# Performance work log

Hardware: AMD Instinct MI355X
Metric: run time of the kernel (lower is better)

## Reference

```python
import jax, jax.numpy as jnp
import numpy as np

TAU = 0.07
EPS = 1e-6  # torch CosineSimilarity eps


def setup_inputs() -> dict:
    key = jax.random.key(0)
    k1, k2, k3 = jax.random.split(key, 3)
    n, d, n_classes = 8192, 256, 1024
    imitation_embeds = jax.random.normal(k1, (n, d), dtype=jnp.float32)
    recording_embeds = jax.random.normal(k2, (n, d), dtype=jnp.float32)
    labels = jax.random.randint(k3, (n,), 0, n_classes, dtype=jnp.int64)
    return {
        "imitation_embeds": imitation_embeds,
        "recording_embeds": recording_embeds,
        "labels": labels,
    }


def reference(imitation_embeds, recording_embeds, labels):
    n = imitation_embeds.shape[0]
    # cosine similarity with per-vector norm clamp (torch semantics)
    im_n = imitation_embeds / jnp.maximum(
        jnp.linalg.norm(imitation_embeds, axis=1, keepdims=True), EPS)
    rec_n = recording_embeds / jnp.maximum(
        jnp.linalg.norm(recording_embeds, axis=1, keepdims=True), EPS)
    i2r = jnp.einsum("nd,md->nm", im_n, rec_n) / TAU  # [n, n]

    same = labels[:, None] == labels[None, :]          # [n, n] bool
    eye = jnp.eye(n, dtype=bool)
    # original: mask = ~(same ^ diag_embed(diag(same))); diag(same) is all True
    # -> keep the diagonal (positive) and all different-label negatives
    mask = ~(same ^ eye)

    # per-row masked log-softmax evaluated at the diagonal entry:
    # log_softmax(row[mask])[pos_of_diag] = i2r[i,i] - logsumexp(row over mask)
    lse = jax.nn.logsumexp(jnp.where(mask, i2r, -jnp.inf), axis=1)  # [n]
    loss = -jnp.mean(jnp.diagonal(i2r) - lse)
    return loss
```

## Files before the change

### kernel.cpp

```cpp
#include <hip/hip_runtime.h>

#define N 8192
#define D 256
#define INV_TAU 14.285714285714286f
#define LOG2E 1.4426950408889634f
#define EPSN 1e-6f

#define RT 256
#define CT 64
#define CSPLIT 16
#define CPB (N / CSPLIT)
#define NTILES (CPB / CT)
#define MAXC 96

typedef unsigned int u32x4 __attribute__((ext_vector_type(4)));
typedef __bf16 bf16x8 __attribute__((ext_vector_type(8)));
typedef float f32x4 __attribute__((ext_vector_type(4)));

__device__ inline unsigned short f2bf(float x) {
    unsigned int u = __builtin_bit_cast(unsigned int, x);
    u += 0x7fffu + ((u >> 16) & 1u);
    return (unsigned short)(u >> 16);
}

__device__ inline float bf2f(unsigned short u) {
    return __builtin_bit_cast(float, (unsigned int)u << 16);
}

__global__ void ntx_prep(const float* __restrict__ im, const float* __restrict__ rec,
                         unsigned short* __restrict__ A, unsigned short* __restrict__ Bm,
                         float* __restrict__ diag, float* __restrict__ rowsum,
                         int* __restrict__ cnt, float* __restrict__ out) {
    const int wave = threadIdx.x >> 6;
    const int lane = threadIdx.x & 63;
    const int row  = blockIdx.x * 4 + wave;

    const float4 a = ((const float4*)(im  + (size_t)row * D))[lane];
    const float4 b = ((const float4*)(rec + (size_t)row * D))[lane];

    float ssa = a.x*a.x + a.y*a.y + a.z*a.z + a.w*a.w;
    float ssb = b.x*b.x + b.y*b.y + b.z*b.z + b.w*b.w;
    float dt  = a.x*b.x + a.y*b.y + a.z*b.z + a.w*b.w;
    #pragma unroll
    for (int o = 32; o; o >>= 1) {
        ssa += __shfl_xor(ssa, o);
        ssb += __shfl_xor(ssb, o);
        dt  += __shfl_xor(dt , o);
    }
    const float ra = 1.0f / fmaxf(sqrtf(ssa), EPSN);
    const float rb = 1.0f / fmaxf(sqrtf(ssb), EPSN);
    const float sa = ra * (INV_TAU * LOG2E);

    ushort4 pa, pb;
    pa.x = f2bf(a.x*sa); pa.y = f2bf(a.y*sa); pa.z = f2bf(a.z*sa); pa.w = f2bf(a.w*sa);
    pb.x = f2bf(b.x*rb); pb.y = f2bf(b.y*rb); pb.z = f2bf(b.z*rb); pb.w = f2bf(b.w*rb);
    *(ushort4*)(A  + (size_t)row * D + lane * 4) = pa;
    *(ushort4*)(Bm + (size_t)row * D + lane * 4) = pb;

    if (lane == 0) {
        diag[row]   = dt * ra * rb * INV_TAU;
        rowsum[row] = 0.0f;
    }
    if (blockIdx.x < 4) cnt[blockIdx.x * 256 + threadIdx.x] = 0;
    if (blockIdx.x == 0 && threadIdx.x == 0) out[0] = 0.0f;
}

__global__ void ntx_bucket(const int* __restrict__ labels, int* __restrict__ cnt,
                           int* __restrict__ bucket) {
    const int i = blockIdx.x * 256 + threadIdx.x;
    const int c = labels[i];
    const int pos = atomicAdd(&cnt[c], 1);
    if (pos < MAXC) bucket[c * MAXC + pos] = i;
}

__global__ void ntx_pairs(const unsigned short* __restrict__ A,
                          const unsigned short* __restrict__ Bm,
                          const int* __restrict__ labels,
                          const int* __restrict__ cnt, const int* __restrict__ bucket,
                          float* __restrict__ rowsum) {
    const int wave = threadIdx.x >> 6;
    const int lane = threadIdx.x & 63;
    const int i = blockIdx.x * 4 + wave;
    const int c = labels[i];
    const int m = min(cnt[c], MAXC);
    if (m < 2) return;

    const ushort4 av = *(const ushort4*)(A + (size_t)i * D + lane * 4);
    const float a0 = bf2f(av.x), a1 = bf2f(av.y), a2 = bf2f(av.z), a3 = bf2f(av.w);

    int jr_n = bucket[c * MAXC];
    ushort4 bv_n = *(const ushort4*)(Bm + (size_t)jr_n * D + lane * 4);

    float corr = 0.f;
    for (int j = 0; j < m; ++j) {
        const int jr = jr_n;
        const ushort4 bv = bv_n;
        if (j + 1 < m) {
            jr_n = bucket[c * MAXC + j + 1];
            bv_n = *(const ushort4*)(Bm + (size_t)jr_n * D + lane * 4);
        }
        if (jr == i) continue;
        float d = a0*bf2f(bv.x) + a1*bf2f(bv.y) + a2*bf2f(bv.z) + a3*bf2f(bv.w);
        #pragma unroll
        for (int o = 32; o; o >>= 1) d += __shfl_xor(d, o);
        corr += __builtin_amdgcn_exp2f(d);
    }
    if (lane == 0) atomicAdd(&rowsum[i], -corr);
}

__device__ __forceinline__ void stage_tile(const unsigned short* gs, unsigned char* lb) {
    #pragma unroll
    for (int p = 0; p < 8; ++p)
        __builtin_amdgcn_global_load_lds(
            (const __attribute__((address_space(1))) unsigned int*)(gs + p * 32),
            (__attribute__((address_space(3))) unsigned int*)(lb + p * 1024),
            16, 0, 0);
}

__global__ __launch_bounds__(256, 2)
void ntx_lse(const unsigned short* __restrict__ A, const unsigned short* __restrict__ Bm,
             float* __restrict__ rowsum) {
    __shared__ __align__(128) unsigned char Bs[2][CT * 512];

    const int wave = threadIdx.x >> 6;
    const int lane = threadIdx.x & 63;
    const int g    = lane >> 4;
    const int n16  = lane & 15;

    const int rowblk = blockIdx.x & (N / RT - 1);
    const int colblk = blockIdx.x >> 5;
    const int row0 = rowblk * RT + wave * 64;
    const int col0 = colblk * CPB;

    bf16x8 afrag[4][8];
    #pragma unroll
    for (int rs = 0; rs < 4; ++rs) {
        const int r = row0 + rs * 16 + n16;
        #pragma unroll
        for (int k = 0; k < 8; ++k)
            afrag[rs][k] = __builtin_bit_cast(
                bf16x8, *(const u32x4*)(A + (size_t)r * D + k * 32 + g * 8));
    }

    float acc[4][4];
    #pragma unroll
    for (int rs = 0; rs < 4; ++rs)
        #pragma unroll
        for (int q = 0; q < 4; ++q) acc[rs][q] = 0.f;

    const unsigned short* gsrc0 = Bm + (size_t)(col0 + wave * 16 + n16) * D + g * 8;
    unsigned char* lds0 = &Bs[0][wave * 8192];
    unsigned char* lds1 = &Bs[1][wave * 8192];

    stage_tile(gsrc0, lds0);
    asm volatile("s_waitcnt vmcnt(0)" ::: "memory");
    __builtin_amdgcn_s_barrier();
    __builtin_amdgcn_sched_barrier(0);

    for (int t = 0; t < NTILES; ++t) {
        const int buf = t & 1;
        if (t + 1 < NTILES)
            stage_tile(gsrc0 + (size_t)(t + 1) * CT * D, buf ? lds0 : lds1);

        #pragma unroll
        for (int cs = 0; cs < 4; ++cs) {
            bf16x8 bfrag[8];
            #pragma unroll
            for (int k = 0; k < 8; ++k)
                bfrag[k] = __builtin_bit_cast(
                    bf16x8, *(const u32x4*)(&Bs[buf][(cs * 8 + k) * 1024 + lane * 16]));

            #pragma unroll
            for (int rs = 0; rs < 4; ++rs) {
                f32x4 c = {0.f, 0.f, 0.f, 0.f};
                #pragma unroll
                for (int k = 0; k < 8; ++k)
                    c = __builtin_amdgcn_mfma_f32_16x16x32_bf16(
                            afrag[rs][k], bfrag[k], c, 0, 0, 0);
                #pragma unroll
                for (int q = 0; q < 4; ++q)
                    acc[rs][q] += __builtin_amdgcn_exp2f(c[q]);
            }
        }

        asm volatile("s_waitcnt vmcnt(0)" ::: "memory");
        __builtin_amdgcn_s_barrier();
        __builtin_amdgcn_sched_barrier(0);
    }

    #pragma unroll
    for (int rs = 0; rs < 4; ++rs)
        #pragma unroll
        for (int q = 0; q < 4; ++q) {
            float v = acc[rs][q];
            v += __shfl_xor(v, 1);
            v += __shfl_xor(v, 2);
            v += __shfl_xor(v, 4);
            v += __shfl_xor(v, 8);
            if (n16 == 0)
                atomicAdd(&rowsum[row0 + rs * 16 + g * 4 + q], v);
        }
}

__global__ void ntx_finish(const float* __restrict__ diag,
                           const float* __restrict__ rowsum,
                           float* __restrict__ out) {
    __shared__ float red[4];
    const int i = blockIdx.x * 256 + threadIdx.x;
    float s = logf(rowsum[i]) - diag[i];
    #pragma unroll
    for (int o = 32; o; o >>= 1) s += __shfl_xor(s, o);
    if ((threadIdx.x & 63) == 0) red[threadIdx.x >> 6] = s;
    __syncthreads();
    if (threadIdx.x == 0)
        atomicAdd(out, (red[0] + red[1] + red[2] + red[3]) * (1.0f / (float)N));
}

extern "C" void kernel_launch(void* const* d_in, const int* in_sizes, int n_in,
                              void* d_out, int out_size, void* d_ws, size_t ws_size,
                              hipStream_t stream) {
    const float* im     = (const float*)d_in[0];
    const float* rec    = (const float*)d_in[1];
    const int*   labels = (const int*)d_in[2];
    float* out = (float*)d_out;

    unsigned short* A  = (unsigned short*)d_ws;
    unsigned short* Bm = A + (size_t)N * D;
    float* diag   = (float*)(Bm + (size_t)N * D);
    float* rowsum = diag + N;
    int*   cnt    = (int*)(rowsum + N);
    int*   bucket = cnt + 1024;

    ntx_prep<<<N / 4, 256, 0, stream>>>(im, rec, A, Bm, diag, rowsum, cnt, out);
    ntx_bucket<<<N / 256, 256, 0, stream>>>(labels, cnt, bucket);
    ntx_pairs<<<N / 4, 256, 0, stream>>>(A, Bm, labels, cnt, bucket, rowsum);
    ntx_lse<<<(N / RT) * CSPLIT, 256, 0, stream>>>(A, Bm, rowsum);
    ntx_finish<<<N / 256, 256, 0, stream>>>(diag, rowsum, out);
}
```

Before: 121.8 us.

## Triple-buffer B tiles with smaller column tiles and interleaved async staging

The LSE GEMM kernel now uses 32-column tiles in a three-buffer LDS ring with two tiles prefetched, waiting with a partial vmcnt instead of draining all loads each iteration. Staging loads are interleaved into the compute sub-steps, all four row-slices' MFMAs are issued before the exp2 accumulation, and s_setprio raises wave priority around the MFMA block. The goal is to hide global-to-LDS latency and overlap matrix work with exponentials. In exchange there are twice as many barriers per column range and the scheduling is more complex.

```diff
diff --git a/kernel.cpp b/kernel.cpp
--- a/kernel.cpp
+++ b/kernel.cpp
@@ -7,7 +7,7 @@
 #define EPSN 1e-6f
 
 #define RT 256
-#define CT 64
+#define CT 32
 #define CSPLIT 16
 #define CPB (N / CSPLIT)
 #define NTILES (CPB / CT)
@@ -108,19 +108,73 @@
     if (lane == 0) atomicAdd(&rowsum[i], -corr);
 }
 
-__device__ __forceinline__ void stage_tile(const unsigned short* gs, unsigned char* lb) {
-    #pragma unroll
-    for (int p = 0; p < 8; ++p)
+__device__ __forceinline__ void stage_tile4(const unsigned short* __restrict__ Bm,
+                                            int colt, int wave, int lane,
+                                            unsigned char* lb) {
+    const int g = lane >> 4, n16 = lane & 15;
+    #pragma unroll
+    for (int p = 0; p < 4; ++p) {
+        const int csk = wave * 4 + p;
+        const int cs = csk >> 3, k = csk & 7;
+        const unsigned short* gs =
+            Bm + (size_t)(colt + cs * 16 + n16) * D + k * 32 + g * 8;
         __builtin_amdgcn_global_load_lds(
-            (const __attribute__((address_space(1))) unsigned int*)(gs + p * 32),
-            (__attribute__((address_space(3))) unsigned int*)(lb + p * 1024),
+            (const __attribute__((address_space(1))) unsigned int*)gs,
+            (__attribute__((address_space(3))) unsigned int*)(lb + csk * 1024),
             16, 0, 0);
+    }
+}
+
+template<bool STAGE>
+__device__ __forceinline__ void tile_step(const unsigned short* __restrict__ Bm,
+                                          int colstage, int wave, int lane,
+                                          const unsigned char* cur, unsigned char* stg,
+                                          const bf16x8 (&afrag)[4][8], float (&acc)[4][4]) {
+    const int g = lane >> 4, n16 = lane & 15;
+    #pragma unroll
+    for (int cs = 0; cs < 2; ++cs) {
+        if constexpr (STAGE) {
+            #pragma unroll
+            for (int p = cs * 2; p < cs * 2 + 2; ++p) {
+                const int csk = wave * 4 + p;
+                const int scs = csk >> 3, sk = csk & 7;
+                const unsigned short* gs =
+                    Bm + (size_t)(colstage + scs * 16 + n16) * D + sk * 32 + g * 8;
+                __builtin_amdgcn_global_load_lds(
+                    (const __attribute__((address_space(1))) unsigned int*)gs,
+                    (__attribute__((address_space(3))) unsigned int*)(stg + csk * 1024),
+                    16, 0, 0);
+            }
+        }
+        bf16x8 bfrag[8];
+        #pragma unroll
+        for (int k = 0; k < 8; ++k)
+            bfrag[k] = __builtin_bit_cast(
+                bf16x8, *(const u32x4*)(cur + (cs * 8 + k) * 1024 + lane * 16));
+
+        f32x4 c[4];
+        __builtin_amdgcn_s_setprio(1);
+        #pragma unroll
+        for (int rs = 0; rs < 4; ++rs) {
+            c[rs] = (f32x4){0.f, 0.f, 0.f, 0.f};
+            #pragma unroll
+            for (int k = 0; k < 8; ++k)
+                c[rs] = __builtin_amdgcn_mfma_f32_16x16x32_bf16(
+                            afrag[rs][k], bfrag[k], c[rs], 0, 0, 0);
+        }
+        __builtin_amdgcn_s_setprio(0);
+        #pragma unroll
+        for (int rs = 0; rs < 4; ++rs)
+            #pragma unroll
+            for (int q = 0; q < 4; ++q)
+                acc[rs][q] += __builtin_amdgcn_exp2f(c[rs][q]);
+    }
 }
 
 __global__ __launch_bounds__(256, 2)
 void ntx_lse(const unsigned short* __restrict__ A, const unsigned short* __restrict__ Bm,
              float* __restrict__ rowsum) {
-    __shared__ __align__(128) unsigned char Bs[2][CT * 512];
+    __shared__ __align__(128) unsigned char Bs[3][CT * 512];
 
     const int wave = threadIdx.x >> 6;
     const int lane = threadIdx.x & 63;
@@ -148,45 +202,29 @@
         #pragma unroll
         for (int q = 0; q < 4; ++q) acc[rs][q] = 0.f;
 
-    const unsigned short* gsrc0 = Bm + (size_t)(col0 + wave * 16 + n16) * D + g * 8;
-    unsigned char* lds0 = &Bs[0][wave * 8192];
-    unsigned char* lds1 = &Bs[1][wave * 8192];
-
-    stage_tile(gsrc0, lds0);
+    unsigned char* b0 = &Bs[0][0];
+    unsigned char* b1 = &Bs[1][0];
+    unsigned char* b2 = &Bs[2][0];
+
+    stage_tile4(Bm, col0,      wave, lane, b0);
+    stage_tile4(Bm, col0 + CT, wave, lane, b1);
+
+    for (int t = 0; t < NTILES - 1; ++t) {
+        asm volatile("s_waitcnt vmcnt(4)" ::: "memory");
+        __builtin_amdgcn_s_barrier();
+        __builtin_amdgcn_sched_barrier(0);
+
+        if (t + 2 < NTILES)
+            tile_step<true >(Bm, col0 + (t + 2) * CT, wave, lane, b0, b2, afrag, acc);
+        else
+            tile_step<false>(Bm, 0, wave, lane, b0, b2, afrag, acc);
+
+        unsigned char* tmp = b0; b0 = b1; b1 = b2; b2 = tmp;
+    }
     asm volatile("s_waitcnt vmcnt(0)" ::: "memory");
     __builtin_amdgcn_s_barrier();
     __builtin_amdgcn_sched_barrier(0);
-
-    for (int t = 0; t < NTILES; ++t) {
-        const int buf = t & 1;
-        if (t + 1 < NTILES)
-            stage_tile(gsrc0 + (size_t)(t + 1) * CT * D, buf ? lds0 : lds1);
-
-        #pragma unroll
-        for (int cs = 0; cs < 4; ++cs) {
-            bf16x8 bfrag[8];
-            #pragma unroll
-            for (int k = 0; k < 8; ++k)
-                bfrag[k] = __builtin_bit_cast(
-                    bf16x8, *(const u32x4*)(&Bs[buf][(cs * 8 + k) * 1024 + lane * 16]));
-
-            #pragma unroll
-            for (int rs = 0; rs < 4; ++rs) {
-                f32x4 c = {0.f, 0.f, 0.f, 0.f};
-                #pragma unroll
-                for (int k = 0; k < 8; ++k)
-                    c = __builtin_amdgcn_mfma_f32_16x16x32_bf16(
-                            afrag[rs][k], bfrag[k], c, 0, 0, 0);
-                #pragma unroll
-                for (int q = 0; q < 4; ++q)
-                    acc[rs][q] += __builtin_amdgcn_exp2f(c[q]);
-            }
-        }
-
-        asm volatile("s_waitcnt vmcnt(0)" ::: "memory");
-        __builtin_amdgcn_s_barrier();
-        __builtin_amdgcn_sched_barrier(0);
-    }
+    tile_step<false>(Bm, 0, wave, lane, b0, b2, afrag, acc);
 
     #pragma unroll
     for (int rs = 0; rs < 4; ++rs)
```

Measured after the change: 121.0 us. No clear change (-0.7%).

## Switch LSE kernel to per-wave double-buffered B tiles without block barriers

Applied to the files above, without the earlier changes.

Each wave now stages its own 16-column B tile into a private double buffer and waits only on its own outstanding loads (vmcnt), so the block-wide barriers after every tile go away. MFMAs are interleaved across the four row subtiles with raised scheduling priority, and the block-to-(row,column) mapping is reordered so neighbouring blocks share column ranges for better L2 reuse. The cost is smaller tiles, more issue overhead per tile, and a reliance on vmcnt ordering being correct for the global_load_lds path.

```diff
diff --git a/kernel.cpp b/kernel.cpp
--- a/kernel.cpp
+++ b/kernel.cpp
@@ -7,10 +7,11 @@
 #define EPSN 1e-6f
 
 #define RT 256
-#define CT 64
+#define CT 16
 #define CSPLIT 16
 #define CPB (N / CSPLIT)
 #define NTILES (CPB / CT)
+#define WTILE (CT * 512)
 #define MAXC 96
 
 typedef unsigned int u32x4 __attribute__((ext_vector_type(4)));
@@ -108,27 +109,67 @@
     if (lane == 0) atomicAdd(&rowsum[i], -corr);
 }
 
-__device__ __forceinline__ void stage_tile(const unsigned short* gs, unsigned char* lb) {
+__device__ __forceinline__ void stage_wtile(const unsigned short* __restrict__ Bm,
+                                            int colt, int lane, unsigned char* buf) {
+    const int g = lane >> 4, n16 = lane & 15;
+    const unsigned short* gs = Bm + (size_t)(colt + n16) * D + g * 8;
     #pragma unroll
     for (int p = 0; p < 8; ++p)
         __builtin_amdgcn_global_load_lds(
             (const __attribute__((address_space(1))) unsigned int*)(gs + p * 32),
-            (__attribute__((address_space(3))) unsigned int*)(lb + p * 1024),
+            (__attribute__((address_space(3))) unsigned int*)(buf + p * 1024),
             16, 0, 0);
+}
+
+template<int W, bool STG>
+__device__ __forceinline__ void wtile_body(const unsigned short* __restrict__ Bm,
+                                           int colstage, int lane, unsigned char* buf,
+                                           const bf16x8 (&afrag)[4][8], float (&acc)[4][4]) {
+    asm volatile("s_waitcnt vmcnt(%0)" :: "n"(W) : "memory");
+    __builtin_amdgcn_sched_barrier(0);
+
+    bf16x8 bf[8];
+    #pragma unroll
+    for (int k = 0; k < 8; ++k)
+        bf[k] = __builtin_bit_cast(
+            bf16x8, *(const u32x4*)(buf + k * 1024 + lane * 16));
+
+    f32x4 c[4];
+    __builtin_amdgcn_s_setprio(1);
+    #pragma unroll
+    for (int k = 0; k < 8; ++k)
+        #pragma unroll
+        for (int rs = 0; rs < 4; ++rs) {
+            if (k == 0) c[rs] = (f32x4){0.f, 0.f, 0.f, 0.f};
+            c[rs] = __builtin_amdgcn_mfma_f32_16x16x32_bf16(
+                        afrag[rs][k], bf[k], c[rs], 0, 0, 0);
+        }
+    __builtin_amdgcn_s_setprio(0);
+
+    #pragma unroll
+    for (int rs = 0; rs < 4; ++rs)
+        #pragma unroll
+        for (int q = 0; q < 4; ++q)
+            acc[rs][q] += __builtin_amdgcn_exp2f(c[rs][q]);
+
+    __builtin_amdgcn_sched_barrier(0);
+    if constexpr (STG) stage_wtile(Bm, colstage, lane, buf);
 }
 
 __global__ __launch_bounds__(256, 2)
 void ntx_lse(const unsigned short* __restrict__ A, const unsigned short* __restrict__ Bm,
              float* __restrict__ rowsum) {
-    __shared__ __align__(128) unsigned char Bs[2][CT * 512];
+    __shared__ __align__(128) unsigned char Bs[4][2][WTILE];
 
     const int wave = threadIdx.x >> 6;
     const int lane = threadIdx.x & 63;
     const int g    = lane >> 4;
     const int n16  = lane & 15;
 
-    const int rowblk = blockIdx.x & (N / RT - 1);
-    const int colblk = blockIdx.x >> 5;
+    const int bid    = blockIdx.x;
+    const int u      = bid >> 3;
+    const int colblk = (bid & 7) | ((u & 1) << 3);
+    const int rowblk = u >> 1;
     const int row0 = rowblk * RT + wave * 64;
     const int col0 = colblk * CPB;
 
@@ -148,45 +189,19 @@
         #pragma unroll
         for (int q = 0; q < 4; ++q) acc[rs][q] = 0.f;
 
-    const unsigned short* gsrc0 = Bm + (size_t)(col0 + wave * 16 + n16) * D + g * 8;
-    unsigned char* lds0 = &Bs[0][wave * 8192];
-    unsigned char* lds1 = &Bs[1][wave * 8192];
-
-    stage_tile(gsrc0, lds0);
-    asm volatile("s_waitcnt vmcnt(0)" ::: "memory");
-    __builtin_amdgcn_s_barrier();
-    __builtin_amdgcn_sched_barrier(0);
-
-    for (int t = 0; t < NTILES; ++t) {
-        const int buf = t & 1;
-        if (t + 1 < NTILES)
-            stage_tile(gsrc0 + (size_t)(t + 1) * CT * D, buf ? lds0 : lds1);
-
-        #pragma unroll
-        for (int cs = 0; cs < 4; ++cs) {
-            bf16x8 bfrag[8];
-            #pragma unroll
-            for (int k = 0; k < 8; ++k)
-                bfrag[k] = __builtin_bit_cast(
-                    bf16x8, *(const u32x4*)(&Bs[buf][(cs * 8 + k) * 1024 + lane * 16]));
-
-            #pragma unroll
-            for (int rs = 0; rs < 4; ++rs) {
-                f32x4 c = {0.f, 0.f, 0.f, 0.f};
-                #pragma unroll
-                for (int k = 0; k < 8; ++k)
-                    c = __builtin_amdgcn_mfma_f32_16x16x32_bf16(
-                            afrag[rs][k], bfrag[k], c, 0, 0, 0);
-                #pragma unroll
-                for (int q = 0; q < 4; ++q)
-                    acc[rs][q] += __builtin_amdgcn_exp2f(c[q]);
-            }
-        }
-
-        asm volatile("s_waitcnt vmcnt(0)" ::: "memory");
-        __builtin_amdgcn_s_barrier();
-        __builtin_amdgcn_sched_barrier(0);
-    }
+    unsigned char* b0 = &Bs[wave][0][0];
+    unsigned char* b1 = &Bs[wave][1][0];
+
+    stage_wtile(Bm, col0 + 0 * CT, lane, b0);
+    stage_wtile(Bm, col0 + 1 * CT, lane, b1);
+
+    #pragma unroll 1
+    for (int t = 0; t < NTILES - 2; t += 2) {
+        wtile_body<8, true >(Bm, col0 + (t + 2) * CT, lane, b0, afrag, acc);
+        wtile_body<8, true >(Bm, col0 + (t + 3) * CT, lane, b1, afrag, acc);
+    }
+    wtile_body<8, false>(Bm, 0, lane, b0, afrag, acc);
+    wtile_body<0, false>(Bm, 0, lane, b1, afrag, acc);
 
     #pragma unroll
     for (int rs = 0; rs < 4; ++rs)
```

Result: slower. 156.2 us (+28.2%).
